# Optimization experiments

Hardware: AMD Instinct MI355X
Metric: run time of the kernel (lower is better)

## Reference

```python
import jax, jax.numpy as jnp
import numpy as np

B, C, H, W = 8, 256, 128, 128
CQK = C // 8  # query/key channels from 1x1 conv
NEG = -jnp.inf


def setup_inputs() -> dict:
    key = jax.random.key(0)
    ks = jax.random.split(key, 9)
    s = 0.05
    return {
        "x1": jax.random.normal(ks[0], (B, C, H, W), jnp.float32),
        "x2": jax.random.normal(ks[1], (B, C, H, W), jnp.float32),
        "Wq": jax.random.normal(ks[2], (CQK, C), jnp.float32) * s,
        "bq": jax.random.normal(ks[3], (CQK,), jnp.float32) * s,
        "Wk": jax.random.normal(ks[4], (CQK, C), jnp.float32) * s,
        "bk": jax.random.normal(ks[5], (CQK,), jnp.float32) * s,
        "Wv": jax.random.normal(ks[6], (C, C), jnp.float32) * s,
        "bv": jax.random.normal(ks[7], (C,), jnp.float32) * s,
        "gamma": jnp.ones((1,), jnp.float32),
    }


def _topk_mask(e, k):
    # keep top-k entries along last axis, set the rest to -inf
    vals = jax.lax.top_k(e, k)[0]
    thr = vals[..., -1:]
    return jnp.where(e >= thr, e, NEG)


def reference(x1, x2, Wq, bq, Wk, bk, Wv, bv, gamma):
    b, c, h, w = x1.shape
    # 1x1 convs == per-pixel linear maps over channels
    q = jnp.einsum('bchw,oc->bohw', x1, Wq) + bq[None, :, None, None]
    k = jnp.einsum('bchw,oc->bohw', x2, Wk) + bk[None, :, None, None]
    v = jnp.einsum('bchw,oc->bohw', x2, Wv) + bv[None, :, None, None]

    # column (H-axis) scores: for pixel (h,w), attend over all h' in same column w
    eH = jnp.einsum('bchw,bcgw->bhwg', q, k)                     # (B,H,W,H)
    eye = jnp.eye(h, dtype=bool)[None, :, None, :]               # mask self on H-axis
    eH = jnp.where(eye, NEG, eH)
    # row (W-axis) scores: attend over all w' in same row h
    eW = jnp.einsum('bchw,bchv->bhwv', q, k)                     # (B,H,W,W)

    # top-k sparsification along each axis (keep top half)
    eH = _topk_mask(eH, h // 2)
    eW = _topk_mask(eW, w // 2)

    att = jax.nn.softmax(jnp.concatenate([eH, eW], axis=-1), axis=-1)  # (B,H,W,H+W)
    attH, attW = att[..., :h], att[..., h:]

    outH = jnp.einsum('bcgw,bhwg->bchw', v, attH)
    outW = jnp.einsum('bchv,bhwv->bchw', v, attW)
    return gamma[0] * (outH + outW) + x1
```

## Files before the change

### kernel.cpp

```cpp
#include <hip/hip_runtime.h>
#include <cstdint>
#include <cstddef>

#define HW 16384
#define NEGF (-__builtin_inff())

typedef unsigned short u16;
typedef _Float16 f16;
typedef _Float16 f16x8 __attribute__((ext_vector_type(8)));
typedef float f32x4 __attribute__((ext_vector_type(4)));

__device__ __forceinline__ unsigned fkey(float f) {
  unsigned b = __float_as_uint(f);
  return (b & 0x80000000u) ? ~b : (b | 0x80000000u);
}
__device__ __forceinline__ float funkey(unsigned u) {
  unsigned b = (u & 0x80000000u) ? (u ^ 0x80000000u) : ~u;
  return __uint_as_float(b);
}

__device__ __forceinline__ float h2f(u16 u) { f16 h; *(u16*)&h = u; return (float)h; }
__device__ __forceinline__ u16 f2h(float f) { f16 h = (f16)f; return *(u16*)&h; }

union i4h8 { int4 i; f16x8 h; };

__global__ __launch_bounds__(256) void pack_kernel(
    const float* __restrict__ Wq, const float* __restrict__ bq,
    const float* __restrict__ Wk, const float* __restrict__ bk,
    const float* __restrict__ Wv, const float* __restrict__ bv,
    u16* __restrict__ Wp, float* __restrict__ ball)
{
  int i = blockIdx.x * 256 + threadIdx.x;
  {
    int chunk = i / 10240;
    int r = i - chunk * 10240;
    int frag = r >> 9;
    int lane = (r >> 3) & 63;
    int j = i & 7;
    int o = frag * 16 + (lane & 15);
    int kk = chunk * 32 + (lane >> 4) * 8 + j;
    float wv_ = (o < 32) ? Wq[o * 256 + kk]
              : (o < 64) ? Wk[(o - 32) * 256 + kk]
                         : Wv[(o - 64) * 256 + kk];
    Wp[i] = f2h(wv_);
  }
  if (i < 320) {
    ball[i] = (i < 32) ? bq[i] : (i < 64) ? bk[i - 32] : bv[i - 64];
  }
}

__global__ __launch_bounds__(256) void proj_kernel(
    const float* __restrict__ x1, const float* __restrict__ x2,
    const u16* __restrict__ Wp, const float* __restrict__ ball,
    u16* __restrict__ q16, u16* __restrict__ k16, u16* __restrict__ v)
{
  __shared__ __align__(16) u16 wlds[10240];
  __shared__ __align__(16) u16 xlds[2][2048];
  const int t = threadIdx.x;
  const int w = t >> 6, l = t & 63;
  const int blk = blockIdx.x;
  const int b = blk >> 8;
  const int p0 = (blk & 255) << 6;

  f32x4 acc[5][4];
#pragma unroll
  for (int f = 0; f < 5; ++f) {
    f32x4 binit;
#pragma unroll
    for (int r = 0; r < 4; ++r)
      binit[r] = ball[(w * 5 + f) * 16 + (l >> 4) * 4 + r];
#pragma unroll
    for (int pf = 0; pf < 4; ++pf) acc[f][pf] = binit;
  }

  const float* xp = (w & 1) ? x2 : x1;
  const int ks_l = (w >> 1) * 16 + (l >> 5) * 8;
  const int px_w = (l & 31) * 2;
  char* xdst = (char*)&xlds[w & 1][0];
  const int kgw = ks_l >> 3;
  const int offA = px_w * 64 + ((kgw ^ (px_w & 3)) << 4);
  const int offB = (px_w + 1) * 64 + ((kgw ^ ((px_w + 1) & 3)) << 4);

  const int prow = l & 15, kg2 = l >> 4;
  const char* xsrc1 = (const char*)&xlds[0][0];
  const char* xsrc2 = (const char*)&xlds[1][0];

  for (int ch = 0; ch < 8; ++ch) {
    int4 wreg[5];
#pragma unroll
    for (int r = 0; r < 5; ++r)
      wreg[r] = *(const int4*)((const char*)Wp + ch * 20480 + (r * 256 + t) * 16);
    float2 xv[8];
    {
      size_t gbase = ((size_t)(b * 256 + ch * 32 + ks_l)) * HW + p0 + px_w;
#pragma unroll
      for (int i = 0; i < 8; ++i) xv[i] = *(const float2*)&xp[gbase + (size_t)i * HW];
    }
    __syncthreads();
#pragma unroll
    for (int r = 0; r < 5; ++r)
      *(int4*)((char*)wlds + (r * 256 + t) * 16) = wreg[r];
    {
      union { u16 h[8]; int4 v4; } pk0, pk1;
#pragma unroll
      for (int i = 0; i < 8; ++i) {
        pk0.h[i] = f2h(xv[i].x); pk1.h[i] = f2h(xv[i].y);
      }
      *(int4*)(xdst + offA) = pk0.v4;
      *(int4*)(xdst + offB) = pk1.v4;
    }
    __syncthreads();

    f16x8 af[5];
#pragma unroll
    for (int f = 0; f < 5; ++f)
      af[f] = *(const f16x8*)((const char*)wlds + (((w * 5 + f) * 64 + l) << 4));
    f16x8 bf[4];
#pragma unroll
    for (int pf = 0; pf < 4; ++pf) {
      int row = pf * 16 + prow;
      bf[pf] = *(const f16x8*)(xsrc2 + row * 64 + ((kg2 ^ (row & 3)) << 4));
    }
    if (w == 0) {
#pragma unroll
      for (int f = 2; f < 5; ++f)
#pragma unroll
        for (int pf = 0; pf < 4; ++pf)
          acc[f][pf] = __builtin_amdgcn_mfma_f32_16x16x32_f16(af[f], bf[pf], acc[f][pf], 0, 0, 0);
#pragma unroll
      for (int pf = 0; pf < 4; ++pf) {
        int row = pf * 16 + prow;
        bf[pf] = *(const f16x8*)(xsrc1 + row * 64 + ((kg2 ^ (row & 3)) << 4));
      }
#pragma unroll
      for (int f = 0; f < 2; ++f)
#pragma unroll
        for (int pf = 0; pf < 4; ++pf)
          acc[f][pf] = __builtin_amdgcn_mfma_f32_16x16x32_f16(af[f], bf[pf], acc[f][pf], 0, 0, 0);
    } else {
#pragma unroll
      for (int f = 0; f < 5; ++f)
#pragma unroll
        for (int pf = 0; pf < 4; ++pf)
          acc[f][pf] = __builtin_amdgcn_mfma_f32_16x16x32_f16(af[f], bf[pf], acc[f][pf], 0, 0, 0);
    }
  }

#pragma unroll
  for (int f = 0; f < 5; ++f) {
    int of = w * 5 + f;
    if (of < 4) {
      u16* dst16 = (of < 2) ? q16 : k16;
      int o = (of & 1) * 16 + (l >> 4) * 4;
#pragma unroll
      for (int pf = 0; pf < 4; ++pf) {
        int px = p0 + pf * 16 + (l & 15);
        ushort4 h4;
        h4.x = f2h(acc[f][pf][0]);
        h4.y = f2h(acc[f][pf][1]);
        h4.z = f2h(acc[f][pf][2]);
        h4.w = f2h(acc[f][pf][3]);
        *(ushort4*)&dst16[((size_t)b * HW + px) * 32 + o] = h4;
      }
    } else {
#pragma unroll
      for (int r = 0; r < 4; ++r) {
        int o = (of - 4) * 16 + (l >> 4) * 4 + r;
        u16* dst = v + ((size_t)b * 256 + o) * HW + (size_t)p0 + (l & 15);
#pragma unroll
        for (int pf = 0; pf < 4; ++pf) dst[pf * 16] = f2h(acc[f][pf][r]);
      }
    }
  }
}

__global__ __launch_bounds__(256) void transpose_b16(
    const u16* __restrict__ in, u16* __restrict__ out)
{
  __shared__ u16 s[32][33];
  const int plane = blockIdx.y;
  const int tw = blockIdx.x & 3, th = blockIdx.x >> 2;
  const u16* ip = in + (size_t)plane * HW;
  u16* op = out + (size_t)plane * HW;
  const int lx = threadIdx.x & 31, ly = threadIdx.x >> 5;
  const int r0 = th << 5, c0 = tw << 5;
#pragma unroll
  for (int r = 0; r < 4; ++r) s[ly + 8 * r][lx] = ip[(r0 + ly + 8 * r) * 128 + c0 + lx];
  __syncthreads();
#pragma unroll
  for (int r = 0; r < 4; ++r) op[(c0 + ly + 8 * r) * 128 + r0 + lx] = s[lx][ly + 8 * r];
}

__global__ __launch_bounds__(256) void transpose_c32(
    const u16* __restrict__ in, u16* __restrict__ out)
{
  const int b = blockIdx.y;
  const int tw = blockIdx.x & 7, th = blockIdx.x >> 3;
  const int lw = threadIdx.x & 15, lh = threadIdx.x >> 4;
  const int h = th * 16 + lh, wc = tw * 16 + lw;
  const u16* src = in + ((size_t)b * HW + h * 128 + wc) * 32;
  u16* dst = out + ((size_t)b * HW + wc * 128 + h) * 32;
  int4 v0 = *(const int4*)&src[0];
  int4 v1 = *(const int4*)&src[8];
  int4 v2 = *(const int4*)&src[16];
  int4 v3 = *(const int4*)&src[24];
  *(int4*)&dst[0] = v0;  *(int4*)&dst[8] = v1;
  *(int4*)&dst[16] = v2; *(int4*)&dst[24] = v3;
}

__global__ __launch_bounds__(256) void addT_kernel(
    const u16* __restrict__ in, const float* __restrict__ gptr, float* __restrict__ out)
{
  __shared__ float s[32][33];
  const int plane = blockIdx.y;
  const int tw = blockIdx.x & 3, th = blockIdx.x >> 2;
  const float g = gptr[0];
  const u16* ip = in + (size_t)plane * HW;
  float* op = out + (size_t)plane * HW;
  const int lx = threadIdx.x & 31, ly = threadIdx.x >> 5;
  const int r0 = th << 5, c0 = tw << 5;
#pragma unroll
  for (int r = 0; r < 4; ++r) s[ly + 8 * r][lx] = h2f(ip[(r0 + ly + 8 * r) * 128 + c0 + lx]);
  __syncthreads();
#pragma unroll
  for (int r = 0; r < 4; ++r) {
    size_t o = (size_t)(c0 + ly + 8 * r) * 128 + r0 + lx;
    op[o] = op[o] + g * s[lx][ly + 8 * r];
  }
}

__global__ __launch_bounds__(256) void stats_kernel(
    const u16* __restrict__ qp, const u16* __restrict__ kp,
    float* __restrict__ thr_out, float* __restrict__ m_out, float* __restrict__ l_out,
    int diag)
{
  __shared__ float q_s[32][132];
  __shared__ float k_s[32][132];
  __shared__ float e_s[32][132];
  const int t = threadIdx.x;
  const int po = blockIdx.x, b = blockIdx.y;

  const u16* qt = qp + (size_t)(b * 128 + po) * 128 * 32;
  const u16* kt = kp + (size_t)(b * 128 + po) * 128 * 32;
#pragma unroll
  for (int r = 0; r < 2; ++r) {
    int idx = t * 8 + r * 2048;
    int h = idx >> 5, c0 = idx & 31;
    i4h8 qv; qv.i = *(const int4*)&qt[idx];
    i4h8 kv; kv.i = *(const int4*)&kt[idx];
#pragma unroll
    for (int j = 0; j < 8; ++j) {
      q_s[c0 + j][h] = (float)qv.h[j];
      k_s[c0 + j][h] = (float)kv.h[j];
    }
  }
  __syncthreads();

  const int hh = t >> 3;
  const int gg0 = (t & 7) << 4;
  const int wv = t >> 6, ln = t & 63;

  for (int h0 = 0; h0 < 128; h0 += 32) {
    float acc[16];
#pragma unroll
    for (int j = 0; j < 16; ++j) acc[j] = 0.0f;
#pragma unroll
    for (int c = 0; c < 32; ++c) {
      float qv = q_s[c][h0 + hh];
      float4 kv[4];
      kv[0] = *(const float4*)&k_s[c][gg0];
      kv[1] = *(const float4*)&k_s[c][gg0 + 4];
      kv[2] = *(const float4*)&k_s[c][gg0 + 8];
      kv[3] = *(const float4*)&k_s[c][gg0 + 12];
#pragma unroll
      for (int j4 = 0; j4 < 4; ++j4) {
        acc[j4 * 4 + 0] = fmaf(qv, kv[j4].x, acc[j4 * 4 + 0]);
        acc[j4 * 4 + 1] = fmaf(qv, kv[j4].y, acc[j4 * 4 + 1]);
        acc[j4 * 4 + 2] = fmaf(qv, kv[j4].z, acc[j4 * 4 + 2]);
        acc[j4 * 4 + 3] = fmaf(qv, kv[j4].w, acc[j4 * 4 + 3]);
      }
    }
    if (diag) {
      int h = h0 + hh;
#pragma unroll
      for (int j = 0; j < 16; ++j)
        if (gg0 + j == h) acc[j] = NEGF;
    }
#pragma unroll
    for (int j4 = 0; j4 < 4; ++j4)
      *(float4*)&e_s[hh][gg0 + j4 * 4] =
          make_float4(acc[j4 * 4 + 0], acc[j4 * 4 + 1], acc[j4 * 4 + 2], acc[j4 * 4 + 3]);
    __syncthreads();

    for (int rr = 0; rr < 8; ++rr) {
      int row = wv * 8 + rr;
      float e0 = e_s[row][ln], e1 = e_s[row][ln + 64];
      unsigned u0 = fkey(e0), u1 = fkey(e1);
      unsigned uthr = 0u;
      for (int bit = 31; bit >= 0; --bit) {
        unsigned cand = uthr | (1u << bit);
        int cnt = __popcll(__ballot(u0 >= cand)) + __popcll(__ballot(u1 >= cand));
        if (cnt >= 64) uthr = cand;
      }
      unsigned um = u0 > u1 ? u0 : u1;
#pragma unroll
      for (int off = 32; off; off >>= 1) {
        unsigned o = __shfl_xor(um, off);
        um = um > o ? um : o;
      }
      float m = funkey(um);
      float s = ((u0 >= uthr) ? __expf(e0 - m) : 0.0f) +
                ((u1 >= uthr) ? __expf(e1 - m) : 0.0f);
#pragma unroll
      for (int off = 32; off; off >>= 1) s += __shfl_xor(s, off);
      if (ln == 0) {
        size_t idx = ((size_t)b * 128 + po) * 128 + h0 + row;
        thr_out[idx] = __uint_as_float(uthr);
        m_out[idx] = m;
        l_out[idx] = s;
      }
    }
    __syncthreads();
  }
}

template <int DIAG, int FUSE>
__global__ __launch_bounds__(512) void out_mfma(
    const u16* __restrict__ q16, const u16* __restrict__ k16, const u16* __restrict__ vp,
    const float* __restrict__ thr_own, const float* __restrict__ m_own, const float* __restrict__ l_own,
    const float* __restrict__ m_oth, const float* __restrict__ l_oth,
    const float* __restrict__ x1, const float* __restrict__ gptr,
    void* __restrict__ outp_v)
{
  __shared__ __align__(16) u16 q_s[128 * 32];
  __shared__ __align__(16) u16 k_s[128 * 32];
  __shared__ __align__(16) u16 att_s[128 * 128];
  __shared__ float m_s[128], il_s[128];
  __shared__ unsigned ut_s[128];

  const int t = threadIdx.x;
  const int w = t >> 6, l = t & 63;
  const int l15 = l & 15, l4 = l >> 4;
  const int po = blockIdx.x, b = blockIdx.y;

  int4 vld[2][4];
#pragma unroll
  for (int nf = 0; nf < 2; ++nf) {
    int c = w * 32 + nf * 16 + l15;
    size_t vb = ((size_t)(b * 256 + c) * 128 + po) * 128 + l4 * 8;
#pragma unroll
    for (int ks = 0; ks < 4; ++ks)
      vld[nf][ks] = *(const int4*)&vp[vb + ks * 32];
  }

  {
    const u16* qt = q16 + (size_t)(b * 128 + po) * 128 * 32;
    const u16* kt = k16 + (size_t)(b * 128 + po) * 128 * 32;
    *(int4*)&q_s[t * 8] = *(const int4*)&qt[t * 8];
    *(int4*)&k_s[t * 8] = *(const int4*)&kt[t * 8];
  }
  if (t < 128) {
    size_t own = ((size_t)b * 128 + po) * 128 + t;
    size_t oth = ((size_t)b * 128 + t) * 128 + po;
    float ma = m_own[own], la = l_own[own];
    float mb = m_oth[oth], lb = l_oth[oth];
    float m = fmaxf(ma, mb);
    float lsum = la * __expf(ma - m) + lb * __expf(mb - m);
    m_s[t] = m;
    il_s[t] = 1.0f / lsum;
    ut_s[t] = __float_as_uint(thr_own[own]);
  }
  __syncthreads();

  f32x4 eacc[8];
#pragma unroll
  for (int nj = 0; nj < 8; ++nj) eacc[nj] = (f32x4){0.f, 0.f, 0.f, 0.f};
  {
    f16x8 aq = *(const f16x8*)&q_s[(w * 16 + l15) * 32 + l4 * 8];
#pragma unroll
    for (int nj = 0; nj < 8; ++nj) {
      f16x8 bk = *(const f16x8*)&k_s[(nj * 16 + l15) * 32 + l4 * 8];
      eacc[nj] = __builtin_amdgcn_mfma_f32_16x16x32_f16(aq, bk, eacc[nj], 0, 0, 0);
    }
  }

  {
    float mm[4], ii[4];
    unsigned uu[4];
#pragma unroll
    for (int r = 0; r < 4; ++r) {
      int i = w * 16 + l4 * 4 + r;
      mm[r] = m_s[i]; ii[r] = il_s[i]; uu[r] = ut_s[i];
    }
#pragma unroll
    for (int nj = 0; nj < 8; ++nj) {
      int j = nj * 16 + l15;
#pragma unroll
      for (int r = 0; r < 4; ++r) {
        int i = w * 16 + l4 * 4 + r;
        float e = eacc[nj][r];
        float a;
        if (DIAG && i == j) {
          a = 0.0f;
        } else {
          unsigned ue = fkey(e);
          a = (ue >= uu[r]) ? __expf(e - mm[r]) * ii[r] : 0.0f;
        }
        att_s[i * 128 + ((((j >> 3) ^ (i & 15)) << 3) | (j & 7))] = f2h(a);
      }
    }
  }
  __syncthreads();

  f32x4 acc[8][2];
#pragma unroll
  for (int mi = 0; mi < 8; ++mi)
#pragma unroll
    for (int nf = 0; nf < 2; ++nf) acc[mi][nf] = (f32x4){0.f, 0.f, 0.f, 0.f};

#pragma unroll
  for (int ks = 0; ks < 4; ++ks) {
    i4h8 bv0, bv1;
    bv0.i = vld[0][ks];
    bv1.i = vld[1][ks];
#pragma unroll
    for (int mi = 0; mi < 8; ++mi) {
      int i = mi * 16 + l15;
      int s = (ks * 4 + l4) ^ (i & 15);
      f16x8 pa = *(const f16x8*)&att_s[i * 128 + s * 8];
      acc[mi][0] = __builtin_amdgcn_mfma_f32_16x16x32_f16(pa, bv0.h, acc[mi][0], 0, 0, 0);
      acc[mi][1] = __builtin_amdgcn_mfma_f32_16x16x32_f16(pa, bv1.h, acc[mi][1], 0, 0, 0);
    }
  }

  const float g = gptr[0];
#pragma unroll
  for (int mi = 0; mi < 8; ++mi) {
#pragma unroll
    for (int nf = 0; nf < 2; ++nf) {
      int c = w * 32 + nf * 16 + l15;
      int i = mi * 16 + l4 * 4;
      size_t ob = ((size_t)(b * 256 + c) * 128 + po) * 128 + i;
      if (FUSE) {
        float* outp = (float*)outp_v;
        float4 xv = *(const float4*)&x1[ob];
        float4 o;
        o.x = g * acc[mi][nf][0] + xv.x;
        o.y = g * acc[mi][nf][1] + xv.y;
        o.z = g * acc[mi][nf][2] + xv.z;
        o.w = g * acc[mi][nf][3] + xv.w;
        *(float4*)&outp[ob] = o;
      } else {
        u16* outp = (u16*)outp_v;
        ushort4 o;
        o.x = f2h(acc[mi][nf][0]);
        o.y = f2h(acc[mi][nf][1]);
        o.z = f2h(acc[mi][nf][2]);
        o.w = f2h(acc[mi][nf][3]);
        *(ushort4*)&outp[ob] = o;
      }
    }
  }
}

extern "C" void kernel_launch(void* const* d_in, const int* in_sizes, int n_in,
                              void* d_out, int out_size, void* d_ws, size_t ws_size,
                              hipStream_t stream)
{
  const float* x1 = (const float*)d_in[0];
  const float* x2 = (const float*)d_in[1];
  const float* Wq = (const float*)d_in[2];
  const float* bq = (const float*)d_in[3];
  const float* Wk = (const float*)d_in[4];
  const float* bk = (const float*)d_in[5];
  const float* Wv = (const float*)d_in[6];
  const float* bv = (const float*)d_in[7];
  const float* gm = (const float*)d_in[8];
  float* out = (float*)d_out;
  float* ws = (float*)d_ws;

  u16*   Wp    = (u16*)ws;
  float* ball  = ws + 81920;
  u16*   q16   = (u16*)(ws + 82304);
  u16*   k16   = q16 + 4194304;
  u16*   q16T  = k16 + 4194304;
  u16*   k16T  = q16T + 4194304;
  float* stats = (float*)(k16T + 4194304);
  u16*   v     = (u16*)(stats + 786432);
  u16*   vT    = v + 33554432;
  u16*   accH  = v;

  float* thrH = stats;
  float* mH   = stats + 131072;
  float* lH   = stats + 262144;
  float* thrW = stats + 393216;
  float* mW   = stats + 524288;
  float* lW   = stats + 655360;

  pack_kernel<<<320, 256, 0, stream>>>(Wq, bq, Wk, bk, Wv, bv, Wp, ball);
  proj_kernel<<<2048, 256, 0, stream>>>(x1, x2, Wp, ball, q16, k16, v);
  transpose_b16<<<dim3(16, 2048), 256, 0, stream>>>(v, vT);
  transpose_c32<<<dim3(64, 8), 256, 0, stream>>>(q16, q16T);
  transpose_c32<<<dim3(64, 8), 256, 0, stream>>>(k16, k16T);
  stats_kernel<<<dim3(128, 8), 256, 0, stream>>>(q16T, k16T, thrH, mH, lH, 1);
  stats_kernel<<<dim3(128, 8), 256, 0, stream>>>(q16, k16, thrW, mW, lW, 0);
  out_mfma<0, 1><<<dim3(128, 8), 512, 0, stream>>>(
      q16, k16, v, thrW, mW, lW, mH, lH, x1, gm, (void*)out);
  out_mfma<1, 0><<<dim3(128, 8), 512, 0, stream>>>(
      q16T, k16T, vT, thrH, mH, lH, mW, lW, x1, gm, (void*)accH);
  addT_kernel<<<dim3(16, 2048), 256, 0, stream>>>(accH, gm, out);
}
```

Before: 828.4 us.

## Stage kernel epilogues through LDS and fuse both attention outputs in one combine kernel

The projection kernel now writes its q/k/v results into shared memory first, then stores them to global memory as wide contiguous vectors instead of scattered 2-byte writes. Both out_mfma passes now write fp16 partial results through an LDS staging buffer with coalesced 16-byte stores, each in place over its own V input. A new addT2 kernel reads the W and H partials and x1 and writes the final fp32 output in one pass. This replaces the fused fp32 write plus the separate read-modify-write add, cutting global traffic and uncoalesced stores. The cost is extra LDS use and barriers, and the W-path result is now rounded to fp16 before the final sum.

```diff
diff --git a/kernel.cpp b/kernel.cpp
--- a/kernel.cpp
+++ b/kernel.cpp
@@ -54,10 +54,14 @@
     const u16* __restrict__ Wp, const float* __restrict__ ball,
     u16* __restrict__ q16, u16* __restrict__ k16, u16* __restrict__ v)
 {
-  __shared__ __align__(16) u16 wlds[10240];
-  __shared__ __align__(16) u16 xlds[2][2048];
+  __shared__ __align__(16) char smem[42496];
+  u16* wlds = (u16*)smem;
+  u16* xlds0 = (u16*)(smem + 20480);
+  u16* xlds1 = (u16*)(smem + 24576);
+
   const int t = threadIdx.x;
   const int w = t >> 6, l = t & 63;
+  const int l15 = l & 15, l4 = l >> 4;
   const int blk = blockIdx.x;
   const int b = blk >> 8;
   const int p0 = (blk & 255) << 6;
@@ -68,7 +72,7 @@
     f32x4 binit;
 #pragma unroll
     for (int r = 0; r < 4; ++r)
-      binit[r] = ball[(w * 5 + f) * 16 + (l >> 4) * 4 + r];
+      binit[r] = ball[(w * 5 + f) * 16 + l4 * 4 + r];
 #pragma unroll
     for (int pf = 0; pf < 4; ++pf) acc[f][pf] = binit;
   }
@@ -76,14 +80,14 @@
   const float* xp = (w & 1) ? x2 : x1;
   const int ks_l = (w >> 1) * 16 + (l >> 5) * 8;
   const int px_w = (l & 31) * 2;
-  char* xdst = (char*)&xlds[w & 1][0];
+  char* xdst = (char*)((w & 1) ? xlds1 : xlds0);
   const int kgw = ks_l >> 3;
   const int offA = px_w * 64 + ((kgw ^ (px_w & 3)) << 4);
   const int offB = (px_w + 1) * 64 + ((kgw ^ ((px_w + 1) & 3)) << 4);
 
-  const int prow = l & 15, kg2 = l >> 4;
-  const char* xsrc1 = (const char*)&xlds[0][0];
-  const char* xsrc2 = (const char*)&xlds[1][0];
+  const int prow = l15, kg2 = l4;
+  const char* xsrc1 = (const char*)xlds0;
+  const char* xsrc2 = (const char*)xlds1;
 
   for (int ch = 0; ch < 8; ++ch) {
     int4 wreg[5];
@@ -146,31 +150,55 @@
     }
   }
 
+  __syncthreads();
+  u16* vs2 = (u16*)smem;
+  u16* qks = (u16*)(smem + 33280);
 #pragma unroll
   for (int f = 0; f < 5; ++f) {
     int of = w * 5 + f;
-    if (of < 4) {
-      u16* dst16 = (of < 2) ? q16 : k16;
-      int o = (of & 1) * 16 + (l >> 4) * 4;
+    if (of >= 4) {
+      int cb = (of - 4) * 16 + l4 * 4;
 #pragma unroll
       for (int pf = 0; pf < 4; ++pf) {
-        int px = p0 + pf * 16 + (l & 15);
         ushort4 h4;
-        h4.x = f2h(acc[f][pf][0]);
-        h4.y = f2h(acc[f][pf][1]);
-        h4.z = f2h(acc[f][pf][2]);
-        h4.w = f2h(acc[f][pf][3]);
-        *(ushort4*)&dst16[((size_t)b * HW + px) * 32 + o] = h4;
+        h4.x = f2h(acc[f][pf][0]); h4.y = f2h(acc[f][pf][1]);
+        h4.z = f2h(acc[f][pf][2]); h4.w = f2h(acc[f][pf][3]);
+        *(ushort4*)&vs2[(pf * 16 + l15) * 260 + cb] = h4;
       }
     } else {
-#pragma unroll
-      for (int r = 0; r < 4; ++r) {
-        int o = (of - 4) * 16 + (l >> 4) * 4 + r;
-        u16* dst = v + ((size_t)b * 256 + o) * HW + (size_t)p0 + (l & 15);
-#pragma unroll
-        for (int pf = 0; pf < 4; ++pf) dst[pf * 16] = f2h(acc[f][pf][r]);
-      }
-    }
+      int ob = (of & 1) * 16 + l4 * 4;
+      int selo = (of >> 1) * 2304;
+#pragma unroll
+      for (int pf = 0; pf < 4; ++pf) {
+        ushort4 h4;
+        h4.x = f2h(acc[f][pf][0]); h4.y = f2h(acc[f][pf][1]);
+        h4.z = f2h(acc[f][pf][2]); h4.w = f2h(acc[f][pf][3]);
+        *(ushort4*)&qks[selo + (pf * 16 + l15) * 36 + ob] = h4;
+      }
+    }
+  }
+  __syncthreads();
+  {
+    const int c = t;
+    u16* dst = v + ((size_t)b * 256 + c) * HW + p0;
+#pragma unroll
+    for (int g8 = 0; g8 < 8; ++g8) {
+      union { u16 h[8]; int4 i; } u;
+#pragma unroll
+      for (int j = 0; j < 8; ++j) u.h[j] = vs2[(g8 * 8 + j) * 260 + c];
+      *(int4*)&dst[g8 * 8] = u.i;
+    }
+  }
+  if (t < 128) {
+    const int sel = t >> 6, px = t & 63;
+    const unsigned long long* sp =
+        (const unsigned long long*)(qks + sel * 2304 + px * 36);
+    u16* dst = (sel ? k16 : q16) + ((size_t)b * HW + p0 + px) * 32;
+    union { unsigned long long u[8]; int4 i4[4]; } buf;
+#pragma unroll
+    for (int j = 0; j < 8; ++j) buf.u[j] = sp[j];
+#pragma unroll
+    for (int j = 0; j < 4; ++j) *(int4*)&dst[j * 8] = buf.i4[j];
   }
 }
 
@@ -208,27 +236,6 @@
   *(int4*)&dst[16] = v2; *(int4*)&dst[24] = v3;
 }
 
-__global__ __launch_bounds__(256) void addT_kernel(
-    const u16* __restrict__ in, const float* __restrict__ gptr, float* __restrict__ out)
-{
-  __shared__ float s[32][33];
-  const int plane = blockIdx.y;
-  const int tw = blockIdx.x & 3, th = blockIdx.x >> 2;
-  const float g = gptr[0];
-  const u16* ip = in + (size_t)plane * HW;
-  float* op = out + (size_t)plane * HW;
-  const int lx = threadIdx.x & 31, ly = threadIdx.x >> 5;
-  const int r0 = th << 5, c0 = tw << 5;
-#pragma unroll
-  for (int r = 0; r < 4; ++r) s[ly + 8 * r][lx] = h2f(ip[(r0 + ly + 8 * r) * 128 + c0 + lx]);
-  __syncthreads();
-#pragma unroll
-  for (int r = 0; r < 4; ++r) {
-    size_t o = (size_t)(c0 + ly + 8 * r) * 128 + r0 + lx;
-    op[o] = op[o] + g * s[lx][ly + 8 * r];
-  }
-}
-
 __global__ __launch_bounds__(256) void stats_kernel(
     const u16* __restrict__ qp, const u16* __restrict__ kp,
     float* __restrict__ thr_out, float* __restrict__ m_out, float* __restrict__ l_out,
@@ -324,19 +331,21 @@
   }
 }
 
-template <int DIAG, int FUSE>
+template <int DIAG>
 __global__ __launch_bounds__(512) void out_mfma(
     const u16* __restrict__ q16, const u16* __restrict__ k16, const u16* __restrict__ vp,
     const float* __restrict__ thr_own, const float* __restrict__ m_own, const float* __restrict__ l_own,
     const float* __restrict__ m_oth, const float* __restrict__ l_oth,
-    const float* __restrict__ x1, const float* __restrict__ gptr,
-    void* __restrict__ outp_v)
-{
-  __shared__ __align__(16) u16 q_s[128 * 32];
-  __shared__ __align__(16) u16 k_s[128 * 32];
-  __shared__ __align__(16) u16 att_s[128 * 128];
-  __shared__ float m_s[128], il_s[128];
-  __shared__ unsigned ut_s[128];
+    u16* __restrict__ outp)
+{
+  __shared__ __align__(16) char smem[50688];
+  u16* q_s   = (u16*)smem;
+  u16* k_s   = (u16*)(smem + 8192);
+  u16* att_s = (u16*)(smem + 16384);
+  float* m_s = (float*)(smem + 49152);
+  float* il_s = (float*)(smem + 49664);
+  unsigned* ut_s = (unsigned*)(smem + 50176);
+  u16* stage = (u16*)smem;
 
   const int t = threadIdx.x;
   const int w = t >> 6, l = t & 63;
@@ -433,33 +442,78 @@
     }
   }
 
+  __syncthreads();
+#pragma unroll
+  for (int rd = 0; rd < 2; ++rd) {
+    if ((w >> 2) == rd) {
+#pragma unroll
+      for (int mi = 0; mi < 8; ++mi)
+#pragma unroll
+        for (int nf = 0; nf < 2; ++nf) {
+          int cslot = (w & 3) * 32 + nf * 16 + l15;
+          int i = mi * 16 + l4 * 4;
+          ushort4 h4;
+          h4.x = f2h(acc[mi][nf][0]); h4.y = f2h(acc[mi][nf][1]);
+          h4.z = f2h(acc[mi][nf][2]); h4.w = f2h(acc[mi][nf][3]);
+          *(ushort4*)&stage[cslot * 132 + i] = h4;
+        }
+    }
+    __syncthreads();
+    {
+      const int cslot = t >> 2, seg = t & 3;
+      const int c = rd * 128 + cslot;
+      const unsigned long long* sp =
+          (const unsigned long long*)(stage + cslot * 132 + seg * 32);
+      u16* dst = outp + ((size_t)(b * 256 + c) * 128 + po) * 128 + seg * 32;
+      union { unsigned long long u[8]; int4 i4[4]; } buf;
+#pragma unroll
+      for (int j = 0; j < 8; ++j) buf.u[j] = sp[j];
+#pragma unroll
+      for (int j = 0; j < 4; ++j) *(int4*)&dst[j * 8] = buf.i4[j];
+    }
+    if (rd == 0) __syncthreads();
+  }
+}
+
+__global__ __launch_bounds__(256) void addT2_kernel(
+    const u16* __restrict__ accW, const u16* __restrict__ accH,
+    const float* __restrict__ x1, const float* __restrict__ gptr,
+    float* __restrict__ out)
+{
+  __shared__ __align__(16) u16 hs[64][72];
+  const int plane = blockIdx.y;
+  const int th = blockIdx.x >> 1, tw = blockIdx.x & 1;
+  const int h0 = th * 64, w0 = tw * 64;
   const float g = gptr[0];
-#pragma unroll
-  for (int mi = 0; mi < 8; ++mi) {
-#pragma unroll
-    for (int nf = 0; nf < 2; ++nf) {
-      int c = w * 32 + nf * 16 + l15;
-      int i = mi * 16 + l4 * 4;
-      size_t ob = ((size_t)(b * 256 + c) * 128 + po) * 128 + i;
-      if (FUSE) {
-        float* outp = (float*)outp_v;
-        float4 xv = *(const float4*)&x1[ob];
-        float4 o;
-        o.x = g * acc[mi][nf][0] + xv.x;
-        o.y = g * acc[mi][nf][1] + xv.y;
-        o.z = g * acc[mi][nf][2] + xv.z;
-        o.w = g * acc[mi][nf][3] + xv.w;
-        *(float4*)&outp[ob] = o;
-      } else {
-        u16* outp = (u16*)outp_v;
-        ushort4 o;
-        o.x = f2h(acc[mi][nf][0]);
-        o.y = f2h(acc[mi][nf][1]);
-        o.z = f2h(acc[mi][nf][2]);
-        o.w = f2h(acc[mi][nf][3]);
-        *(ushort4*)&outp[ob] = o;
-      }
-    }
+  const int t = threadIdx.x;
+
+  {
+    int wr = t >> 2, seg = t & 3;
+    const u16* src = accH + (size_t)plane * HW + (size_t)(w0 + wr) * 128 + h0 + seg * 16;
+    int4 a = *(const int4*)&src[0];
+    int4 b2 = *(const int4*)&src[8];
+    *(int4*)&hs[wr][seg * 16] = a;
+    *(int4*)&hs[wr][seg * 16 + 8] = b2;
+  }
+  __syncthreads();
+
+  const int h = t & 63, wseg = t >> 6;
+  size_t rbase = (size_t)plane * HW + (size_t)(h0 + h) * 128 + w0 + wseg * 16;
+  const u16* wsrc = accW + rbase;
+  const float* xsrc = x1 + rbase;
+  float* osrc = out + rbase;
+  union { int4 i4[2]; u16 hx[16]; } uw;
+  uw.i4[0] = *(const int4*)&wsrc[0];
+  uw.i4[1] = *(const int4*)&wsrc[8];
+#pragma unroll
+  for (int j4 = 0; j4 < 4; ++j4) {
+    float4 xv = *(const float4*)&xsrc[j4 * 4];
+    float4 o;
+    o.x = g * (h2f(uw.hx[j4 * 4 + 0]) + h2f(hs[wseg * 16 + j4 * 4 + 0][h])) + xv.x;
+    o.y = g * (h2f(uw.hx[j4 * 4 + 1]) + h2f(hs[wseg * 16 + j4 * 4 + 1][h])) + xv.y;
+    o.z = g * (h2f(uw.hx[j4 * 4 + 2]) + h2f(hs[wseg * 16 + j4 * 4 + 2][h])) + xv.z;
+    o.w = g * (h2f(uw.hx[j4 * 4 + 3]) + h2f(hs[wseg * 16 + j4 * 4 + 3][h])) + xv.w;
+    *(float4*)&osrc[j4 * 4] = o;
   }
 }
 
@@ -488,7 +542,6 @@
   float* stats = (float*)(k16T + 4194304);
   u16*   v     = (u16*)(stats + 786432);
   u16*   vT    = v + 33554432;
-  u16*   accH  = v;
 
   float* thrH = stats;
   float* mH   = stats + 131072;
@@ -504,9 +557,9 @@
   transpose_c32<<<dim3(64, 8), 256, 0, stream>>>(k16, k16T);
   stats_kernel<<<dim3(128, 8), 256, 0, stream>>>(q16T, k16T, thrH, mH, lH, 1);
   stats_kernel<<<dim3(128, 8), 256, 0, stream>>>(q16, k16, thrW, mW, lW, 0);
-  out_mfma<0, 1><<<dim3(128, 8), 512, 0, stream>>>(
-      q16, k16, v, thrW, mW, lW, mH, lH, x1, gm, (void*)out);
-  out_mfma<1, 0><<<dim3(128, 8), 512, 0, stream>>>(
-      q16T, k16T, vT, thrH, mH, lH, mW, lW, x1, gm, (void*)accH);
-  addT_kernel<<<dim3(16, 2048), 256, 0, stream>>>(accH, gm, out);
-}
+  out_mfma<0><<<dim3(128, 8), 512, 0, stream>>>(
+      q16, k16, v, thrW, mW, lW, mH, lH, v);
+  out_mfma<1><<<dim3(128, 8), 512, 0, stream>>>(
+      q16T, k16T, vT, thrH, mH, lH, mW, lW, vT);
+  addT2_kernel<<<dim3(4, 2048), 256, 0, stream>>>(v, vT, x1, gm, out);
+}
```

Measured after the change: 837.6 us. Within noise of the previous version (+1.1%).
